# Kernel optimization log

Measured on AMD Instinct MI355X. Metric: run time of the kernel, lower is better.

Reference implementation:

```python
import jax, jax.numpy as jnp
import numpy as np

B, L, E = 256, 500, 300  # bsz, max_doc_len, word_embed_dim
KS = [3, 5, 7]           # filters_size


def setup_inputs() -> dict:
    key = jax.random.key(0)
    ks = jax.random.split(key, 1 + 2 * len(KS))
    inp = {"x": jax.random.normal(ks[0], (B, L, E), jnp.float32)}
    i = 1
    for k in KS:
        # PyTorch Conv2d default init scale ~ 1/sqrt(fan_in)
        inp[f"aw{k}"] = jax.random.normal(ks[i], (k, E), jnp.float32) / np.sqrt(k * E).astype(np.float32); i += 1
        inp[f"ab{k}"] = jnp.zeros((1,), jnp.float32)
        inp[f"cw{k}"] = jax.random.normal(ks[i], (E,), jnp.float32) / np.sqrt(E).astype(np.float32); i += 1
        inp[f"cb{k}"] = jnpp = jnp.zeros((1,), jnp.float32)
    return inp


def _branch(x, aw, ab, cw, cb):
    # x: (B, L, E); aw: (k, E); cw: (E,)
    k = aw.shape[0]
    p = (k - 1) // 2
    x4 = x[:, None, :, :]            # NCHW: (B, 1, L, E)
    w4 = aw[None, None, :, :]        # OIHW: (1, 1, k, E)
    s = jax.lax.conv_general_dilated(x4, w4, window_strides=(1, 1),
                                     padding=((p, p), (0, 0)))  # (B, 1, L, 1)
    score = jax.nn.sigmoid(s + ab[0])[:, 0, :, :]               # (B, L, 1)
    gated = x * score                                           # broadcast over E
    # Conv2d(1,1,(1,E)) == per-timestep dot product over E
    return jnp.tanh(jnp.einsum('ble,e->bl', gated, cw) + cb[0])  # (B, L)


def reference(x, aw3, ab3, cw3, cb3, aw5, ab5, cw5, cb5, aw7, ab7, cw7, cb7):
    return (_branch(x, aw3, ab3, cw3, cb3),
            _branch(x, aw5, ab5, cw5, cb5),
            _branch(x, aw7, ab7, cw7, cb7))
```

## Files before the change

### kernel.cpp

```cpp
#include <hip/hip_runtime.h>
#include <math.h>

#define BB 256
#define LL 500
#define EE 300
#define NROWS (BB * LL)
#define NJ 18
#define NC 75
#define TOUT 56
#define GRP 3
#define NT 3
#define DROWS 64


__device__ __forceinline__ float red16(float v) {
    int t;
    t = __builtin_amdgcn_update_dpp(0, __float_as_int(v), 0xB1, 0xF, 0xF, true);
    v += __int_as_float(t);
    t = __builtin_amdgcn_update_dpp(0, __float_as_int(v), 0x4E, 0xF, 0xF, true);
    v += __int_as_float(t);
    t = __builtin_amdgcn_update_dpp(0, __float_as_int(v), 0x124, 0xF, 0xF, true);
    v += __int_as_float(t);
    t = __builtin_amdgcn_update_dpp(0, __float_as_int(v), 0x128, 0xF, 0xF, true);
    v += __int_as_float(t);
    return v;
}

__device__ __forceinline__ void lds_fence_barrier() {
    asm volatile("s_waitcnt lgkmcnt(0)" ::: "memory");
    __builtin_amdgcn_s_barrier();
    asm volatile("" ::: "memory");
}

__global__ __launch_bounds__(256) void fused_kernel(
    const float* __restrict__ x,
    const float* __restrict__ aw3, const float* __restrict__ ab3,
    const float* __restrict__ cw3, const float* __restrict__ cb3,
    const float* __restrict__ aw5, const float* __restrict__ ab5,
    const float* __restrict__ cw5, const float* __restrict__ cb5,
    const float* __restrict__ aw7, const float* __restrict__ ab7,
    const float* __restrict__ cw7, const float* __restrict__ cb7,
    float* __restrict__ out)
{
    __shared__ float4 wlds[NJ * NC];
    __shared__ float dlds[DROWS][NJ + 1];

    const int tid = threadIdx.x;

    {
        const float4* s3a = (const float4*)aw3;
        const float4* s3c = (const float4*)cw3;
        const float4* s5a = (const float4*)aw5;
        const float4* s5c = (const float4*)cw5;
        const float4* s7a = (const float4*)aw7;
        const float4* s7c = (const float4*)cw7;
        for (int i = tid; i < 225; i += 256) wlds[i]        = s3a[i];
        for (int i = tid; i < 75;  i += 256) wlds[225 + i]  = s3c[i];
        for (int i = tid; i < 375; i += 256) wlds[300 + i]  = s5a[i];
        for (int i = tid; i < 75;  i += 256) wlds[675 + i]  = s5c[i];
        for (int i = tid; i < 525; i += 256) wlds[750 + i]  = s7a[i];
        for (int i = tid; i < 75;  i += 256) wlds[1275 + i] = s7c[i];
    }

    const int b    = blockIdx.x / GRP;
    const int grp  = blockIdx.x % GRP;
    const int wave = tid >> 6;
    const int lane = tid & 63;
    const int g    = lane >> 4;
    const int j    = lane & 15;
    const int lr   = wave * 16 + g * 4;

    const float* xbb = x + (size_t)b * LL * EE;

    float4 xall[5][4];
    {
        const int l0 = (grp * NT) * TOUT - 3;
#pragma unroll
        for (int rr = 0; rr < 4; ++rr) {
            const int l  = l0 + lr + rr;
            const int lc = l < 0 ? 0 : (l >= LL ? LL - 1 : l);
            const float4* xr = (const float4*)(xbb + (size_t)lc * EE);
#pragma unroll
            for (int k = 0; k < 5; ++k) {
                const int c = (k == 4) ? ((j < 11) ? (j + 64) : 74) : (j + 16 * k);
                xall[k][rr] = xr[c];
            }
        }
    }

    lds_fence_barrier();

#pragma unroll 1
    for (int tt = 0; tt < NT; ++tt) {
        const int t  = grp * NT + tt;
        const int l0 = t * TOUT - 3;

        float vf[4];
#pragma unroll
        for (int rr = 0; rr < 4; ++rr) {
            const int l = l0 + lr + rr;
            vf[rr] = (l >= 0 && l < LL) ? 1.0f : 0.0f;
        }

        float acc[NJ][4];
#pragma unroll
        for (int d = 0; d < NJ; ++d)
#pragma unroll
            for (int rr = 0; rr < 4; ++rr) acc[d][rr] = 0.0f;

#define COMPUTE(k, c)                                                               \
    {                                                                               \
        _Pragma("unroll")                                                           \
        for (int d = 0; d < NJ; ++d) {                                              \
            const float4 w = wlds[d * NC + (c)];                                    \
            acc[d][0] = fmaf(xall[k][0].w, w.w, fmaf(xall[k][0].z, w.z, fmaf(xall[k][0].y, w.y, fmaf(xall[k][0].x, w.x, acc[d][0])))); \
            acc[d][1] = fmaf(xall[k][1].w, w.w, fmaf(xall[k][1].z, w.z, fmaf(xall[k][1].y, w.y, fmaf(xall[k][1].x, w.x, acc[d][1])))); \
            acc[d][2] = fmaf(xall[k][2].w, w.w, fmaf(xall[k][2].z, w.z, fmaf(xall[k][2].y, w.y, fmaf(xall[k][2].x, w.x, acc[d][2])))); \
            acc[d][3] = fmaf(xall[k][3].w, w.w, fmaf(xall[k][3].z, w.z, fmaf(xall[k][3].y, w.y, fmaf(xall[k][3].x, w.x, acc[d][3])))); \
        }                                                                           \
    }

        COMPUTE(0, j)
        COMPUTE(1, j + 16)
        COMPUTE(2, j + 32)
        COMPUTE(3, j + 48)
        if (j < 11) {
            COMPUTE(4, j + 64)
        }
#undef COMPUTE

        if (tt + 1 < NT) {
            const int l0n = (t + 1) * TOUT - 3;
#pragma unroll
            for (int rr = 0; rr < 4; ++rr) {
                const int l  = l0n + lr + rr;
                const int lc = l < 0 ? 0 : (l >= LL ? LL - 1 : l);
                const float4* xr = (const float4*)(xbb + (size_t)lc * EE);
#pragma unroll
                for (int k = 0; k < 5; ++k) {
                    const int c = (k == 4) ? ((j < 11) ? (j + 64) : 74) : (j + 16 * k);
                    xall[k][rr] = xr[c];
                }
            }
        }

#pragma unroll
        for (int d = 0; d < NJ; ++d)
#pragma unroll
            for (int rr = 0; rr < 4; ++rr) acc[d][rr] = red16(acc[d][rr]);

#pragma unroll
        for (int rr = 0; rr < 4; ++rr) {
            if (j == rr) {
#pragma unroll
                for (int d = 0; d < NJ; ++d) dlds[lr + rr][d] = acc[d][rr] * vf[rr];
            }
        }

        lds_fence_barrier();

        if (wave < 3 && lane < TOUT) {
            const int lo = t * TOUT + lane;
            if (lo < LL) {
                const int c = lane + 3;
                const int r = b * LL + lo;

                if (wave == 0) {
                    float pre = 0.0f;
#pragma unroll
                    for (int tp = 0; tp < 3; ++tp) pre += dlds[c + tp - 1][tp];
                    const float s = 1.0f / (1.0f + expf(-(pre + ab3[0])));
                    out[r] = tanhf(s * dlds[c][3] + cb3[0]);
                } else if (wave == 1) {
                    float pre = 0.0f;
#pragma unroll
                    for (int tp = 0; tp < 5; ++tp) pre += dlds[c + tp - 2][4 + tp];
                    const float s = 1.0f / (1.0f + expf(-(pre + ab5[0])));
                    out[NROWS + r] = tanhf(s * dlds[c][9] + cb5[0]);
                } else {
                    float pre = 0.0f;
#pragma unroll
                    for (int tp = 0; tp < 7; ++tp) pre += dlds[c + tp - 3][10 + tp];
                    const float s = 1.0f / (1.0f + expf(-(pre + ab7[0])));
                    out[2 * NROWS + r] = tanhf(s * dlds[c][17] + cb7[0]);
                }
            }
        }

        lds_fence_barrier();
    }
}

extern "C" void kernel_launch(void* const* d_in, const int* in_sizes, int n_in,
                              void* d_out, int out_size, void* d_ws, size_t ws_size,
                              hipStream_t stream) {
    const float* x   = (const float*)d_in[0];
    const float* aw3 = (const float*)d_in[1];
    const float* ab3 = (const float*)d_in[2];
    const float* cw3 = (const float*)d_in[3];
    const float* cb3 = (const float*)d_in[4];
    const float* aw5 = (const float*)d_in[5];
    const float* ab5 = (const float*)d_in[6];
    const float* cw5 = (const float*)d_in[7];
    const float* cb5 = (const float*)d_in[8];
    const float* aw7 = (const float*)d_in[9];
    const float* ab7 = (const float*)d_in[10];
    const float* cw7 = (const float*)d_in[11];
    const float* cb7 = (const float*)d_in[12];

    float* out = (float*)d_out;

    fused_kernel<<<BB * GRP, 256, 0, stream>>>(
        x, aw3, ab3, cw3, cb3, aw5, ab5, cw5, cb5, aw7, ab7, cw7, cb7, out);
}
```

Before: 246.7 us.

## Make each wave process independent 10-output jobs with a private LDS scratch

After: 282.6 us. +14.5%, slower.

```diff
diff --git a/kernel.cpp b/kernel.cpp
--- a/kernel.cpp
+++ b/kernel.cpp
@@ -7,10 +7,10 @@
 #define NROWS (BB * LL)
 #define NJ 18
 #define NC 75
-#define TOUT 56
-#define GRP 3
-#define NT 3
-#define DROWS 64
+#define OPJ 10
+#define NJOBS 50
+#define JPW 4
+#define WROWS 16
 
 
 __device__ __forceinline__ float red16(float v) {
@@ -43,7 +43,7 @@
     float* __restrict__ out)
 {
     __shared__ float4 wlds[NJ * NC];
-    __shared__ float dlds[DROWS][NJ + 1];
+    __shared__ float dlds[4][WROWS][NJ + 1];
 
     const int tid = threadIdx.x;
 
@@ -62,19 +62,20 @@
         for (int i = tid; i < 75;  i += 256) wlds[1275 + i] = s7c[i];
     }
 
-    const int b    = blockIdx.x / GRP;
-    const int grp  = blockIdx.x % GRP;
-    const int wave = tid >> 6;
-    const int lane = tid & 63;
-    const int g    = lane >> 4;
-    const int j    = lane & 15;
-    const int lr   = wave * 16 + g * 4;
-
-    const float* xbb = x + (size_t)b * LL * EE;
+    const int batch = blockIdx.x >> 2;
+    const int sub   = blockIdx.x & 3;
+    const int wave  = tid >> 6;
+    const int lane  = tid & 63;
+    const int g     = lane >> 4;
+    const int j     = lane & 15;
+    const int lr    = g * 4;
+    const int job0  = sub * 16 + wave * JPW;
+
+    const float* xbb = x + (size_t)batch * LL * EE;
 
     float4 xall[5][4];
-    {
-        const int l0 = (grp * NT) * TOUT - 3;
+    if (job0 < NJOBS) {
+        const int l0 = job0 * OPJ - 3;
 #pragma unroll
         for (int rr = 0; rr < 4; ++rr) {
             const int l  = l0 + lr + rr;
@@ -89,11 +90,15 @@
     }
 
     lds_fence_barrier();
+    if (job0 >= NJOBS) return;
+
+    float* dl = &dlds[wave][0][0];
 
 #pragma unroll 1
-    for (int tt = 0; tt < NT; ++tt) {
-        const int t  = grp * NT + tt;
-        const int l0 = t * TOUT - 3;
+    for (int jj = 0; jj < JPW; ++jj) {
+        const int job = job0 + jj;
+        if (job >= NJOBS) break;
+        const int l0 = job * OPJ - 3;
 
         float vf[4];
 #pragma unroll
@@ -129,8 +134,8 @@
         }
 #undef COMPUTE
 
-        if (tt + 1 < NT) {
-            const int l0n = (t + 1) * TOUT - 3;
+        if (jj + 1 < JPW && job + 1 < NJOBS) {
+            const int l0n = (job + 1) * OPJ - 3;
 #pragma unroll
             for (int rr = 0; rr < 4; ++rr) {
                 const int l  = l0n + lr + rr;
@@ -153,41 +158,37 @@
         for (int rr = 0; rr < 4; ++rr) {
             if (j == rr) {
 #pragma unroll
-                for (int d = 0; d < NJ; ++d) dlds[lr + rr][d] = acc[d][rr] * vf[rr];
-            }
-        }
-
-        lds_fence_barrier();
-
-        if (wave < 3 && lane < TOUT) {
-            const int lo = t * TOUT + lane;
-            if (lo < LL) {
-                const int c = lane + 3;
-                const int r = b * LL + lo;
-
-                if (wave == 0) {
-                    float pre = 0.0f;
-#pragma unroll
-                    for (int tp = 0; tp < 3; ++tp) pre += dlds[c + tp - 1][tp];
-                    const float s = 1.0f / (1.0f + expf(-(pre + ab3[0])));
-                    out[r] = tanhf(s * dlds[c][3] + cb3[0]);
-                } else if (wave == 1) {
-                    float pre = 0.0f;
-#pragma unroll
-                    for (int tp = 0; tp < 5; ++tp) pre += dlds[c + tp - 2][4 + tp];
-                    const float s = 1.0f / (1.0f + expf(-(pre + ab5[0])));
-                    out[NROWS + r] = tanhf(s * dlds[c][9] + cb5[0]);
-                } else {
-                    float pre = 0.0f;
-#pragma unroll
-                    for (int tp = 0; tp < 7; ++tp) pre += dlds[c + tp - 3][10 + tp];
-                    const float s = 1.0f / (1.0f + expf(-(pre + ab7[0])));
-                    out[2 * NROWS + r] = tanhf(s * dlds[c][17] + cb7[0]);
-                }
-            }
-        }
-
-        lds_fence_barrier();
+                for (int d = 0; d < NJ; ++d) dl[(lr + rr) * (NJ + 1) + d] = acc[d][rr] * vf[rr];
+            }
+        }
+
+        asm volatile("s_waitcnt lgkmcnt(0)" ::: "memory");
+
+        if (lane < OPJ) {
+            const int c = lane + 3;
+            const int r = batch * LL + job * OPJ + lane;
+            {
+                float pre = 0.0f;
+#pragma unroll
+                for (int tp = 0; tp < 3; ++tp) pre += dl[(c + tp - 1) * (NJ + 1) + tp];
+                const float s = 1.0f / (1.0f + expf(-(pre + ab3[0])));
+                out[r] = tanhf(s * dl[c * (NJ + 1) + 3] + cb3[0]);
+            }
+            {
+                float pre = 0.0f;
+#pragma unroll
+                for (int tp = 0; tp < 5; ++tp) pre += dl[(c + tp - 2) * (NJ + 1) + 4 + tp];
+                const float s = 1.0f / (1.0f + expf(-(pre + ab5[0])));
+                out[NROWS + r] = tanhf(s * dl[c * (NJ + 1) + 9] + cb5[0]);
+            }
+            {
+                float pre = 0.0f;
+#pragma unroll
+                for (int tp = 0; tp < 7; ++tp) pre += dl[(c + tp - 3) * (NJ + 1) + 10 + tp];
+                const float s = 1.0f / (1.0f + expf(-(pre + ab7[0])));
+                out[2 * NROWS + r] = tanhf(s * dl[c * (NJ + 1) + 17] + cb7[0]);
+            }
+        }
     }
 }
 
@@ -210,6 +211,6 @@
 
     float* out = (float*)d_out;
 
-    fused_kernel<<<BB * GRP, 256, 0, stream>>>(
+    fused_kernel<<<BB * 4, 256, 0, stream>>>(
         x, aw3, ab3, cw3, cb3, aw5, ab5, cw5, cb5, aw7, ab7, cw7, cb7, out);
 }
```
